# Kernel optimization log

Hardware: AMD Instinct MI355X
Metric: run time of the kernel (lower is better)

Reference implementation:

```python
import jax, jax.numpy as jnp
import numpy as np

B_, T_, N_, C_ = 8, 24, 207, 128      # batch, time (fixed 24), nodes (fixed 207), channels
RED = C_ // 2                          # reducted_size = 64 (Mamba d_model)
DIN = 2 * RED                          # Mamba d_inner (expand=2) = 128
DS, DCONV, DTR = 16, 4, 4              # d_state, d_conv, dt_rank = ceil(64/16)


def _ln(x, w, b, eps=1e-5):
    m = jnp.mean(x, -1, keepdims=True)
    v = jnp.mean((x - m) ** 2, -1, keepdims=True)
    return (x - m) * jax.lax.rsqrt(v + eps) * w + b


def _causal_conv(x, w, b):
    # depthwise causal conv along seq; x: (B,L,D), w: (D,K)
    K = w.shape[1]
    L = x.shape[1]
    xp = jnp.pad(x, ((0, 0), (K - 1, 0), (0, 0)))
    return sum(xp[:, k:k + L, :] * w[:, k] for k in range(K)) + b


def _mamba(h, inproj, conv_w, conv_b, xproj, dtw, dtb, Alog, Dp, outproj):
    # mamba_ssm Mamba(d_model=RED) forward, eval mode
    xz = h @ inproj                                        # (B,L,2*DIN)
    u, z = jnp.split(xz, 2, axis=-1)
    u = jax.nn.silu(_causal_conv(u, conv_w, conv_b))       # (B,L,DIN)
    xdbl = u @ xproj                                       # (B,L,DTR+2*DS)
    dt = jax.nn.softplus(xdbl[..., :DTR] @ dtw + dtb)      # (B,L,DIN)
    Bm = xdbl[..., DTR:DTR + DS]                           # (B,L,DS)
    Cm = xdbl[..., DTR + DS:]                              # (B,L,DS)
    A = -jnp.exp(Alog)                                     # (DIN,DS)

    def step(hs, inp):
        dt_t, B_t, C_t, u_t = inp                          # (B,DIN),(B,DS),(B,DS),(B,DIN)
        hs = hs * jnp.exp(dt_t[..., None] * A) + (dt_t * u_t)[..., None] * B_t[:, None, :]
        return hs, jnp.einsum('bdn,bn->bd', hs, C_t)

    h0 = jnp.zeros((u.shape[0], DIN, DS), u.dtype)
    xs = (dt.swapaxes(0, 1), Bm.swapaxes(0, 1), Cm.swapaxes(0, 1), u.swapaxes(0, 1))
    _, ys = jax.lax.scan(step, h0, xs)                     # (L,B,DIN)
    y = ys.swapaxes(0, 1) + u * Dp
    y = y * jax.nn.silu(z)
    return y @ outproj                                     # (B,L,RED)


def setup_inputs() -> dict:
    key = jax.random.key(0)
    ks = iter(jax.random.split(key, 64))

    def rn(shape, s):
        return jax.random.normal(next(ks), shape, jnp.float32) * s

    inp = {
        "x": jax.random.normal(next(ks), (B_, T_, N_, C_), jnp.float32),
        "qk": jax.random.normal(next(ks), (B_, T_, N_, C_), jnp.float32),
        "in_ln_w": jnp.ones(2 * C_), "in_ln_b": jnp.zeros(2 * C_),
        "in_w": rn((2 * C_, RED), 0.05), "in_b": jnp.zeros(RED),
        "ov_ln_w": jnp.ones(RED), "ov_ln_b": jnp.zeros(RED),
        "ov_w": rn((RED, C_), 0.05), "ov_b": jnp.zeros(C_),
        "o_ln_w": jnp.ones(C_), "o_ln_b": jnp.zeros(C_),
        "o_w": rn((C_, C_), 0.05), "o_b": jnp.zeros(C_),
    }
    for p in ("fw", "bw"):
        inp[p + "_inproj"] = rn((RED, 2 * DIN), 0.05)
        inp[p + "_conv_w"] = rn((DIN, DCONV), 0.2)
        inp[p + "_conv_b"] = jnp.zeros(DIN)
        inp[p + "_xproj"] = rn((DIN, DTR + 2 * DS), 0.05)
        inp[p + "_dtw"] = rn((DTR, DIN), 0.2)
        dt0 = jnp.exp(jax.random.uniform(next(ks), (DIN,)) * (np.log(0.1) - np.log(1e-3)) + np.log(1e-3))
        inp[p + "_dtb"] = jnp.log(jnp.expm1(dt0))          # inverse softplus (mamba dt init)
        inp[p + "_Alog"] = jnp.log(jnp.broadcast_to(jnp.arange(1, DS + 1, dtype=jnp.float32), (DIN, DS)))
        inp[p + "_D"] = jnp.ones(DIN)
        inp[p + "_outproj"] = rn((DIN, RED), 0.05)
    return inp


def reference(x, qk, in_ln_w, in_ln_b, in_w, in_b,
              fw_inproj, fw_conv_w, fw_conv_b, fw_xproj, fw_dtw, fw_dtb, fw_Alog, fw_D, fw_outproj,
              bw_inproj, bw_conv_w, bw_conv_b, bw_xproj, bw_dtw, bw_dtb, bw_Alog, bw_D, bw_outproj,
              ov_ln_w, ov_ln_b, ov_w, ov_b, o_ln_w, o_ln_b, o_w, o_b):
    x_in = x
    h = jnp.concatenate([x, qk], -1).reshape(B_ * T_, N_, 2 * C_)   # 'b t n f -> (b t) n f'
    h = _ln(h, in_ln_w, in_ln_b) @ in_w + in_b                       # (B*T, N, RED)
    h_fw = _mamba(h, fw_inproj, fw_conv_w, fw_conv_b, fw_xproj, fw_dtw, fw_dtb, fw_Alog, fw_D, fw_outproj)
    h_bw = _mamba(h[:, ::-1], bw_inproj, bw_conv_w, bw_conv_b, bw_xproj, bw_dtw, bw_dtb, bw_Alog, bw_D, bw_outproj)[:, ::-1]
    h = h_fw + h_bw
    h = _ln(h, ov_ln_w, ov_ln_b) @ ov_w + ov_b                       # dropout: eval no-op
    h = h.reshape(B_, T_, N_, C_) + x_in                             # '(b t) n f -> b t n f' + residual
    return _ln(h, o_ln_w, o_ln_b) @ o_w + o_b
```

## Files before the change

kernel.cpp:

```cpp
#include <hip/hip_runtime.h>
#include <hip/hip_bf16.h>

#define B__ 8
#define T__ 24
#define N__ 207
#define C__ 128
#define BT_ 192
#define L__ 207
#define RED_ 64
#define DIN_ 128
#define DS_ 16
#define DTR_ 4
#define XD_ 36
#define NC_ 6
#define CHK_ 35
#define NROW_ 39744

#define P_OVLNW 0
#define P_OVLNB 64
#define P_OVB   128
#define P_OLNW  256
#define P_OLNB  384
#define P_OB    512
#define P_INB   640
#define P_LNW   704
#define P_LNB   960
#define P_TOT   1216

using bf16 = __hip_bfloat16;

typedef __attribute__((ext_vector_type(8))) short bf8v;
typedef __attribute__((ext_vector_type(4))) short s4v;
typedef __attribute__((ext_vector_type(4))) float f4v;

__device__ __forceinline__ float ldin(const void* __restrict__ p, int i, int md) {
    if (md) return ((const float*)p)[i];
    return __bfloat162float(((const bf16*)p)[i]);
}
__device__ __forceinline__ float ldbf(const bf16* __restrict__ p, int i) {
    return __bfloat162float(p[i]);
}

__device__ __forceinline__ short f2bf(float f) {
    unsigned u = __builtin_bit_cast(unsigned, f);
    unsigned r = (u + 0x7FFFu + ((u >> 16) & 1u)) >> 16;
    return (short)(unsigned short)r;
}
__device__ __forceinline__ float bfl(short h) {
    return __builtin_bit_cast(float, ((unsigned)(unsigned short)h) << 16);
}

__global__ void k0_detect(const void* __restrict__ lnw, int* __restrict__ mode,
                          int* __restrict__ geo) {
    unsigned short h0 = ((const unsigned short*)lnw)[0];
    *mode = (h0 == 0x3F80u) ? 0 : 1;
    *geo  = 1;
}

__global__ void probe_order_dict() {}
__global__ void probe_order_signature() {}

__global__ __launch_bounds__(256) void k_prep(
    const void* __restrict__ op_fw, const void* __restrict__ op_bw,
    const void* __restrict__ ovw, const void* __restrict__ ow,
    const void* __restrict__ ovlnw, const void* __restrict__ ovlnb,
    const void* __restrict__ ovb,
    const void* __restrict__ olnw, const void* __restrict__ olnb,
    const void* __restrict__ ob,
    const void* __restrict__ inw, const void* __restrict__ inb,
    const void* __restrict__ inlnw, const void* __restrict__ inlnb,
    const void* __restrict__ ipj_fw, const void* __restrict__ ipj_bw,
    const void* __restrict__ cw_fw, const void* __restrict__ cb_fw,
    const void* __restrict__ cw_bw, const void* __restrict__ cb_bw,
    const void* __restrict__ xp_fw, const void* __restrict__ xp_bw,
    const void* __restrict__ Alog_fw, const void* __restrict__ Alog_bw,
    short* __restrict__ w0t_hi, short* __restrict__ w0t_lo,
    short* __restrict__ w2t_hi, short* __restrict__ w2t_lo,
    short* __restrict__ w1t_hi, short* __restrict__ w1t_lo,
    short* __restrict__ ovwt_hi, short* __restrict__ ovwt_lo,
    short* __restrict__ owt_hi, short* __restrict__ owt_lo,
    short* __restrict__ w3t_hi, short* __restrict__ w3t_lo,
    float* __restrict__ cwt, float* __restrict__ cbt,
    float* __restrict__ pars, const int* __restrict__ mode,
    int* __restrict__ geo)
{
    const int md = *mode;
    const int stride = gridDim.x * blockDim.x;
    const int t0 = blockIdx.x * blockDim.x + threadIdx.x;
    for (int i = t0; i < 64*256; i += stride) {
        int c = i >> 8, k = i & 255;
        float wv = ldin(inw, k*64 + c, md);
        short h = f2bf(wv); w0t_hi[i] = h; w0t_lo[i] = f2bf(wv - bfl(h));
    }
    for (int i = t0; i < 2*256*64; i += stride) {
        int dir = i >> 14, c = (i >> 6) & 255, k = i & 63;
        const void* src = dir ? ipj_bw : ipj_fw;
        float wv = ldin(src, k*256 + c, md);
        short h = f2bf(wv); w2t_hi[i] = h; w2t_lo[i] = f2bf(wv - bfl(h));
    }
    for (int i = t0; i < 64*256; i += stride) {
        int c = i >> 8, k = i & 255;
        float wv = (k < 128) ? ldin(op_fw, k*64 + c, md)
                             : ldin(op_bw, (k-128)*64 + c, md);
        short h = f2bf(wv); w1t_hi[i] = h; w1t_lo[i] = f2bf(wv - bfl(h));
    }
    for (int i = t0; i < 128*64; i += stride) {
        int c = i >> 6, k = i & 63;
        float wv = ldin(ovw, k*128 + c, md);
        short h = f2bf(wv); ovwt_hi[i] = h; ovwt_lo[i] = f2bf(wv - bfl(h));
    }
    for (int i = t0; i < 128*128; i += stride) {
        int c = i >> 7, k = i & 127;
        float wv = ldin(ow, k*128 + c, md);
        short h = f2bf(wv); owt_hi[i] = h; owt_lo[i] = f2bf(wv - bfl(h));
    }
    for (int i = t0; i < 2*48*128; i += stride) {
        int dir = i / 6144, rem = i % 6144;
        int c = rem >> 7, k = rem & 127;
        float wv = (c < XD_) ? ldin(dir ? xp_bw : xp_fw, k*XD_ + c, md) : 0.f;
        short h = f2bf(wv); w3t_hi[i] = h; w3t_lo[i] = f2bf(wv - bfl(h));
    }
    for (int i = t0; i < 2*4*128; i += stride) {
        int dir = i >> 9, k = (i >> 7) & 3, d = i & 127;
        cwt[i] = ldin(dir ? cw_bw : cw_fw, d*4 + k, md);
    }
    for (int i = t0; i < 2*128; i += stride) {
        int dir = i >> 7, d = i & 127;
        cbt[i] = ldin(dir ? cb_bw : cb_fw, d, md);
    }
    for (int i = t0; i < 2*DIN_*DS_; i += stride) {
        int dir = i >> 11, rem = i & 2047;
        int d = rem >> 4, s = rem & 15;
        const void* Al = dir ? Alog_bw : Alog_fw;
        float A  = -__expf(ldin(Al, d*DS_ + s, md));
        float A0 = -__expf(ldin(Al, d*DS_ + 0, md));
        float tgt = (float)(s + 1) * A0;
        float tol = 1e-4f * fabsf(tgt) + 1e-6f;
        if (fabsf(A - tgt) > tol) atomicAnd(geo, 0);
    }
    for (int i = t0; i < P_TOT; i += stride) {
        float v;
        if      (i < 64)   v = ldin(ovlnw, i,        md);
        else if (i < 128)  v = ldin(ovlnb, i-64,     md);
        else if (i < 256)  v = ldin(ovb,   i-128,    md);
        else if (i < 384)  v = ldin(olnw,  i-256,    md);
        else if (i < 512)  v = ldin(olnb,  i-384,    md);
        else if (i < 640)  v = ldin(ob,    i-512,    md);
        else if (i < 704)  v = ldin(inb,   i-640,    md);
        else if (i < 960)  v = ldin(inlnw, i-704,    md);
        else               v = ldin(inlnb, i-960,    md);
        pars[i] = v;
    }
}

__global__ __launch_bounds__(64) void k1_mfma(
    const void* __restrict__ x, const void* __restrict__ qk,
    const short* __restrict__ w0t_hi, const short* __restrict__ w0t_lo,
    const float* __restrict__ pars,
    bf16* __restrict__ hbuf, const int* __restrict__ mode)
{
    const int md  = *mode;
    const int l   = threadIdx.x;
    const int lg  = l >> 4;
    const int lc  = l & 15;
    const int wrow = blockIdx.x * 16;
    const int r = wrow + lc;
    const int cb = lg * 32;

    __shared__ __align__(16) short t0h[16][272];
    __shared__ __align__(16) short t0l[16][272];

    const f4v zero = {0.f, 0.f, 0.f, 0.f};

    if (md) {
        float4 vx[8], vq[8];
        const float* spx = (const float*)x  + (size_t)r * C__ + cb;
        const float* spq = (const float*)qk + (size_t)r * C__ + cb;
#pragma unroll
        for (int t = 0; t < 8; ++t) {
            vx[t] = *reinterpret_cast<const float4*>(spx + 4*t);
            vq[t] = *reinterpret_cast<const float4*>(spq + 4*t);
        }
        float s = 0.f, ss = 0.f;
#pragma unroll
        for (int t = 0; t < 8; ++t) {
            s  += vx[t].x + vx[t].y + vx[t].z + vx[t].w
                + vq[t].x + vq[t].y + vq[t].z + vq[t].w;
            ss += vx[t].x*vx[t].x + vx[t].y*vx[t].y + vx[t].z*vx[t].z + vx[t].w*vx[t].w
                + vq[t].x*vq[t].x + vq[t].y*vq[t].y + vq[t].z*vq[t].z + vq[t].w*vq[t].w;
        }
        s  += __shfl_xor(s, 16, 64);  ss += __shfl_xor(ss, 16, 64);
        s  += __shfl_xor(s, 32, 64);  ss += __shfl_xor(ss, 32, 64);
        const float mean = s * (1.f/256.f);
        const float rs   = rsqrtf(ss * (1.f/256.f) - mean*mean + 1e-5f);
#pragma unroll
        for (int t = 0; t < 8; ++t) {
            float vv[4] = {vx[t].x, vx[t].y, vx[t].z, vx[t].w};
            s4v hi, lo;
#pragma unroll
            for (int e = 0; e < 4; ++e) {
                int gc = cb + 4*t + e;
                float a = (vv[e] - mean) * rs * pars[P_LNW + gc] + pars[P_LNB + gc];
                short h = f2bf(a); hi[e] = h; lo[e] = f2bf(a - bfl(h));
            }
            *reinterpret_cast<s4v*>(&t0h[lc][cb + 4*t]) = hi;
            *reinterpret_cast<s4v*>(&t0l[lc][cb + 4*t]) = lo;
        }
#pragma unroll
        for (int t = 0; t < 8; ++t) {
            float vv[4] = {vq[t].x, vq[t].y, vq[t].z, vq[t].w};
            s4v hi, lo;
#pragma unroll
            for (int e = 0; e < 4; ++e) {
                int gc = 128 + cb + 4*t + e;
                float a = (vv[e] - mean) * rs * pars[P_LNW + gc] + pars[P_LNB + gc];
                short h = f2bf(a); hi[e] = h; lo[e] = f2bf(a - bfl(h));
            }
            *reinterpret_cast<s4v*>(&t0h[lc][128 + cb + 4*t]) = hi;
            *reinterpret_cast<s4v*>(&t0l[lc][128 + cb + 4*t]) = lo;
        }
    } else {
        bf8v vx[4], vq[4];
        const short* spx = (const short*)x  + (size_t)r * C__ + cb;
        const short* spq = (const short*)qk + (size_t)r * C__ + cb;
#pragma unroll
        for (int t = 0; t < 4; ++t) {
            vx[t] = *reinterpret_cast<const bf8v*>(spx + 8*t);
            vq[t] = *reinterpret_cast<const bf8v*>(spq + 8*t);
        }
        float s = 0.f, ss = 0.f;
#pragma unroll
        for (int t = 0; t < 4; ++t)
#pragma unroll
            for (int e = 0; e < 8; ++e) {
                float fx = bfl(vx[t][e]); s += fx; ss += fx*fx;
                float fq = bfl(vq[t][e]); s += fq; ss += fq*fq;
            }
        s  += __shfl_xor(s, 16, 64);  ss += __shfl_xor(ss, 16, 64);
        s  += __shfl_xor(s, 32, 64);  ss += __shfl_xor(ss, 32, 64);
        const float mean = s * (1.f/256.f);
        const float rs   = rsqrtf(ss * (1.f/256.f) - mean*mean + 1e-5f);
#pragma unroll
        for (int t = 0; t < 4; ++t)
#pragma unroll
            for (int hh = 0; hh < 2; ++hh) {
                s4v hi, lo;
#pragma unroll
                for (int e = 0; e < 4; ++e) {
                    int gc = cb + 8*t + 4*hh + e;
                    float a = (bfl(vx[t][4*hh+e]) - mean) * rs * pars[P_LNW + gc] + pars[P_LNB + gc];
                    short h = f2bf(a); hi[e] = h; lo[e] = f2bf(a - bfl(h));
                }
                *reinterpret_cast<s4v*>(&t0h[lc][cb + 8*t + 4*hh]) = hi;
                *reinterpret_cast<s4v*>(&t0l[lc][cb + 8*t + 4*hh]) = lo;
            }
#pragma unroll
        for (int t = 0; t < 4; ++t)
#pragma unroll
            for (int hh = 0; hh < 2; ++hh) {
                s4v hi, lo;
#pragma unroll
                for (int e = 0; e < 4; ++e) {
                    int gc = 128 + cb + 8*t + 4*hh + e;
                    float a = (bfl(vq[t][4*hh+e]) - mean) * rs * pars[P_LNW + gc] + pars[P_LNB + gc];
                    short h = f2bf(a); hi[e] = h; lo[e] = f2bf(a - bfl(h));
                }
                *reinterpret_cast<s4v*>(&t0h[lc][128 + cb + 8*t + 4*hh]) = hi;
                *reinterpret_cast<s4v*>(&t0l[lc][128 + cb + 8*t + 4*hh]) = lo;
            }
    }

    f4v acc1[4];
#pragma unroll
    for (int nt = 0; nt < 4; ++nt) acc1[nt] = zero;

#pragma unroll
    for (int p = 0; p < 2; ++p) {
#pragma unroll
        for (int kk = 0; kk < 4; ++kk) {
            bf8v ah = *reinterpret_cast<const bf8v*>(&t0h[lc][p*128 + kk*32 + lg*8]);
            bf8v al = *reinterpret_cast<const bf8v*>(&t0l[lc][p*128 + kk*32 + lg*8]);
#pragma unroll
            for (int nt = 0; nt < 4; ++nt) {
                const int bo = (nt*16 + lc)*256 + p*128 + kk*32 + lg*8;
                bf8v bh = *reinterpret_cast<const bf8v*>(w0t_hi + bo);
                bf8v bl = *reinterpret_cast<const bf8v*>(w0t_lo + bo);
                acc1[nt] = __builtin_amdgcn_mfma_f32_16x16x32_bf16(ah, bl, acc1[nt], 0, 0, 0);
                acc1[nt] = __builtin_amdgcn_mfma_f32_16x16x32_bf16(al, bh, acc1[nt], 0, 0, 0);
                acc1[nt] = __builtin_amdgcn_mfma_f32_16x16x32_bf16(ah, bh, acc1[nt], 0, 0, 0);
            }
        }
    }

    short* hp = (short*)hbuf;
#pragma unroll
    for (int nt = 0; nt < 4; ++nt)
#pragma unroll
        for (int j = 0; j < 4; ++j)
            hp[(size_t)(wrow + lg*4 + j)*RED_ + nt*16 + lc] =
                f2bf(acc1[nt][j] + pars[P_INB + nt*16 + lc]);
}

__global__ __launch_bounds__(64) void k2_mfma(
    const bf16* __restrict__ hbuf,
    const short* __restrict__ w2t_hi, const short* __restrict__ w2t_lo,
    bf16* __restrict__ uraw, bf16* __restrict__ zbuf)
{
    const int l   = threadIdx.x;
    const int lg  = l >> 4;
    const int lc  = l & 15;
    const int wrow = blockIdx.x * 16;
    const int dir  = blockIdx.y >> 1;
    const int nh   = blockIdx.y & 1;

    const short* hp = (const short*)hbuf + (size_t)(wrow + lc) * RED_;
    bf8v ha0 = *reinterpret_cast<const bf8v*>(hp + lg*8);
    bf8v ha1 = *reinterpret_cast<const bf8v*>(hp + 32 + lg*8);

    const f4v zero = {0.f, 0.f, 0.f, 0.f};
    const int g0 = wrow + lg*4;
    const int qg = g0 / 207, ng0 = g0 - qg * 207;

    f4v acc2[8];
#pragma unroll
    for (int nt = 0; nt < 8; ++nt) acc2[nt] = zero;
#pragma unroll
    for (int nt = 0; nt < 8; ++nt) {
        const int ntg = nh*8 + nt;
        const int co = dir*16384 + (ntg*16 + lc)*64;
        bf8v bh0 = *reinterpret_cast<const bf8v*>(w2t_hi + co + lg*8);
        bf8v bl0 = *reinterpret_cast<const bf8v*>(w2t_lo + co + lg*8);
        bf8v bh1 = *reinterpret_cast<const bf8v*>(w2t_hi + co + 32 + lg*8);
        bf8v bl1 = *reinterpret_cast<const bf8v*>(w2t_lo + co + 32 + lg*8);
        acc2[nt] = __builtin_amdgcn_mfma_f32_16x16x32_bf16(ha0, bl0, acc2[nt], 0, 0, 0);
        acc2[nt] = __builtin_amdgcn_mfma_f32_16x16x32_bf16(ha0, bh0, acc2[nt], 0, 0, 0);
        acc2[nt] = __builtin_amdgcn_mfma_f32_16x16x32_bf16(ha1, bl1, acc2[nt], 0, 0, 0);
        acc2[nt] = __builtin_amdgcn_mfma_f32_16x16x32_bf16(ha1, bh1, acc2[nt], 0, 0, 0);
    }
    bf16* __restrict__ dst = nh ? zbuf : uraw;
#pragma unroll
    for (int j = 0; j < 4; ++j) {
        int ng = ng0 + j, qq = qg;
        if (ng >= 207) { ng -= 207; ++qq; }
        const int ro = dir ? ((192 + qq)*207 + (206 - ng)) : (qq*207 + ng);
#pragma unroll
        for (int nt = 0; nt < 8; ++nt) {
            const int c = nt*16 + lc;
            dst[(size_t)ro*DIN_ + c] = __float2bfloat16(acc2[nt][j]);
        }
    }
}

__global__ __launch_bounds__(64) void k34_mfma(
    const bf16* __restrict__ uraw,
    const float* __restrict__ cwt, const float* __restrict__ cbt,
    const short* __restrict__ w3t_hi, const short* __restrict__ w3t_lo,
    bf16* __restrict__ ubuf, float* __restrict__ xdbl)
{
    const int l   = threadIdx.x;
    const int lg  = l >> 4;
    const int lc  = l & 15;
    const int wrow = blockIdx.x * 16;
    const int dir  = wrow / NROW_;
    const int r    = wrow + lc;
    const int m    = (r - dir * NROW_) % 207;

    __shared__ __align__(16) short uhh[16][136];
    __shared__ __align__(16) short ull[16][136];

    const float* __restrict__ cw = cwt + dir * 512;
    const float* __restrict__ cb = cbt + dir * 128;
    const int c0 = lg * 32;

#pragma unroll
    for (int t = 0; t < 4; ++t) {
        const int cc = c0 + t*8;
        float s[8];
#pragma unroll
        for (int e = 0; e < 8; ++e) s[e] = cb[cc + e];
#pragma unroll
        for (int k = 0; k < 3; ++k) {
            if (m - 3 + k >= 0) {
                bf8v v = *reinterpret_cast<const bf8v*>(
                    (const short*)uraw + (size_t)(r - 3 + k)*DIN_ + cc);
#pragma unroll
                for (int e = 0; e < 8; ++e) s[e] += bfl(v[e]) * cw[k*128 + cc + e];
            }
        }
        {
            bf8v v = *reinterpret_cast<const bf8v*>(
                (const short*)uraw + (size_t)r*DIN_ + cc);
#pragma unroll
            for (int e = 0; e < 8; ++e) s[e] += bfl(v[e]) * cw[3*128 + cc + e];
        }
        s4v h0, h1, l0, l1;
        bf8v uo;
#pragma unroll
        for (int e = 0; e < 8; ++e) {
            float u = s[e] / (1.f + __expf(-s[e]));
            short h = f2bf(u);
            short lo = f2bf(u - bfl(h));
            uo[e] = h;
            if (e < 4) { h0[e] = h; l0[e] = lo; }
            else       { h1[e-4] = h; l1[e-4] = lo; }
        }
        *reinterpret_cast<s4v*>(&uhh[lc][cc])     = h0;
        *reinterpret_cast<s4v*>(&uhh[lc][cc + 4]) = h1;
        *reinterpret_cast<s4v*>(&ull[lc][cc])     = l0;
        *reinterpret_cast<s4v*>(&ull[lc][cc + 4]) = l1;
        *reinterpret_cast<bf8v*>((short*)ubuf + (size_t)r*DIN_ + cc) = uo;
    }

    const f4v zero = {0.f, 0.f, 0.f, 0.f};
    f4v acc[3];
#pragma unroll
    for (int nt = 0; nt < 3; ++nt) acc[nt] = zero;
    const int wb = dir * 6144;
#pragma unroll
    for (int kk = 0; kk < 4; ++kk) {
        bf8v ah = *reinterpret_cast<const bf8v*>(&uhh[lc][kk*32 + lg*8]);
        bf8v al = *reinterpret_cast<const bf8v*>(&ull[lc][kk*32 + lg*8]);
#pragma unroll
        for (int nt = 0; nt < 3; ++nt) {
            const int bo = wb + (nt*16 + lc)*128 + kk*32 + lg*8;
            bf8v bh = *reinterpret_cast<const bf8v*>(w3t_hi + bo);
            bf8v bl = *reinterpret_cast<const bf8v*>(w3t_lo + bo);
            acc[nt] = __builtin_amdgcn_mfma_f32_16x16x32_bf16(ah, bl, acc[nt], 0, 0, 0);
            acc[nt] = __builtin_amdgcn_mfma_f32_16x16x32_bf16(al, bh, acc[nt], 0, 0, 0);
            acc[nt] = __builtin_amdgcn_mfma_f32_16x16x32_bf16(ah, bh, acc[nt], 0, 0, 0);
        }
    }
#pragma unroll
    for (int nt = 0; nt < 3; ++nt) {
        const int c = nt*16 + lc;
        if (c < XD_) {
#pragma unroll
            for (int j = 0; j < 4; ++j)
                xdbl[(size_t)(wrow + lg*4 + j)*XD_ + c] = acc[nt][j];
        }
    }
}

__global__ __launch_bounds__(128) void k5a_local(
    const float* __restrict__ xdbl,
    const bf16* __restrict__ ubuf,
    float* __restrict__ h_end, float* __restrict__ sumdt,
    const void* __restrict__ dtw_fw, const void* __restrict__ dtb_fw,
    const void* __restrict__ Alog_fw,
    const void* __restrict__ dtw_bw, const void* __restrict__ dtb_bw,
    const void* __restrict__ Alog_bw,
    const int* __restrict__ mode, const int* __restrict__ geo)
{
    const int md = *mode;
    const int c = blockIdx.x, q = blockIdx.y, dir = blockIdx.z;
    const int d = threadIdx.x;
    const void* __restrict__ dtw  = dir ? dtw_bw  : dtw_fw;
    const void* __restrict__ dtbp = dir ? dtb_bw  : dtb_fw;
    const void* __restrict__ Alog = dir ? Alog_bw : Alog_fw;
    const float w0 = ldin(dtw, 0*DIN_ + d, md), w1 = ldin(dtw, 1*DIN_ + d, md);
    const float w2 = ldin(dtw, 2*DIN_ + d, md), w3 = ldin(dtw, 3*DIN_ + d, md);
    const float dtb = ldin(dtbp, d, md);
    float st[DS_];
#pragma unroll
    for (int s = 0; s < DS_; ++s) st[s] = 0.f;
    float sdt = 0.f;
    const int seq = dir*BT_ + q;
    const int m0 = c * CHK_;
    if (*geo) {
        const float A0 = -__expf(ldin(Alog, d*DS_ + 0, md));
        for (int m = m0; m < m0 + CHK_; ++m) {
            const float* __restrict__ xd = xdbl + (seq*L__ + m)*XD_;
            float4 xt = *reinterpret_cast<const float4*>(xd);
            float dtp = xt.x*w0 + xt.y*w1 + xt.z*w2 + xt.w*w3 + dtb;
            float dt = (dtp > 15.f) ? dtp : __logf(1.f + __expf(dtp));
            sdt += dt;
            float u = ldbf(ubuf, (seq*L__ + m)*DIN_ + d);
            float du = dt * u;
            float bb[DS_];
#pragma unroll
            for (int t = 0; t < 4; ++t) {
                float4 v = *reinterpret_cast<const float4*>(xd + DTR_ + 4*t);
                bb[4*t] = v.x; bb[4*t+1] = v.y; bb[4*t+2] = v.z; bb[4*t+3] = v.w;
            }
            float e1 = __expf(dt * A0);
            float pw = 1.f;
#pragma unroll
            for (int s = 0; s < DS_; ++s) {
                pw *= e1;
                st[s] = st[s]*pw + du*bb[s];
            }
        }
    } else {
        float A[DS_];
#pragma unroll
        for (int s = 0; s < DS_; ++s) A[s] = -__expf(ldin(Alog, d*DS_ + s, md));
        for (int m = m0; m < m0 + CHK_; ++m) {
            const float* __restrict__ xd = xdbl + (seq*L__ + m)*XD_;
            float4 xt = *reinterpret_cast<const float4*>(xd);
            float dtp = xt.x*w0 + xt.y*w1 + xt.z*w2 + xt.w*w3 + dtb;
            float dt = (dtp > 15.f) ? dtp : log1pf(__expf(dtp));
            sdt += dt;
            float u = ldbf(ubuf, (seq*L__ + m)*DIN_ + d);
            float du = dt * u;
            float bb[DS_];
#pragma unroll
            for (int t = 0; t < 4; ++t) {
                float4 v = *reinterpret_cast<const float4*>(xd + DTR_ + 4*t);
                bb[4*t] = v.x; bb[4*t+1] = v.y; bb[4*t+2] = v.z; bb[4*t+3] = v.w;
            }
#pragma unroll
            for (int s = 0; s < DS_; ++s)
                st[s] = st[s]*__expf(dt*A[s]) + du*bb[s];
        }
    }
    float* __restrict__ he = h_end + (size_t)(seq*5 + c)*(DIN_*DS_) + d*DS_;
#pragma unroll
    for (int t = 0; t < 4; ++t) {
        float4 v; v.x = st[4*t]; v.y = st[4*t+1]; v.z = st[4*t+2]; v.w = st[4*t+3];
        *reinterpret_cast<float4*>(he + 4*t) = v;
    }
    sumdt[(seq*5 + c)*DIN_ + d] = sdt;
}

__global__ __launch_bounds__(128) void k5c_scan(
    const float* __restrict__ xdbl,
    const bf16* __restrict__ zbuf,
    bf16* __restrict__ ubuf,
    const float* __restrict__ h_end, const float* __restrict__ sumdt,
    const void* __restrict__ dtw_fw, const void* __restrict__ dtb_fw,
    const void* __restrict__ Alog_fw, const void* __restrict__ D_fw,
    const void* __restrict__ dtw_bw, const void* __restrict__ dtb_bw,
    const void* __restrict__ Alog_bw, const void* __restrict__ D_bw,
    const int* __restrict__ mode, const int* __restrict__ geo)
{
    const int md = *mode;
    const int c = blockIdx.x, q = blockIdx.y, dir = blockIdx.z;
    const int d = threadIdx.x;
    const void* __restrict__ dtw  = dir ? dtw_bw  : dtw_fw;
    const void* __restrict__ dtbp = dir ? dtb_bw  : dtb_fw;
    const void* __restrict__ Alog = dir ? Alog_bw : Alog_fw;
    const void* __restrict__ Dp   = dir ? D_bw    : D_fw;
    const float w0 = ldin(dtw, 0*DIN_ + d, md), w1 = ldin(dtw, 1*DIN_ + d, md);
    const float w2 = ldin(dtw, 2*DIN_ + d, md), w3 = ldin(dtw, 3*DIN_ + d, md);
    const float dtb = ldin(dtbp, d, md), Dv = ldin(Dp, d, md);
    const int seq = dir*BT_ + q;
    const int m0 = c * CHK_;
    const int m1 = (m0 + CHK_ < L__) ? (m0 + CHK_) : L__;

    float st[DS_];
#pragma unroll
    for (int s = 0; s < DS_; ++s) st[s] = 0.f;

    if (*geo) {
        const float A0 = -__expf(ldin(Alog, d*DS_ + 0, md));
        for (int j = 0; j < c; ++j) {
            float sd = sumdt[(seq*5 + j)*DIN_ + d];
            const float* __restrict__ he = h_end + (size_t)(seq*5 + j)*(DIN_*DS_) + d*DS_;
            float hv[DS_];
#pragma unroll
            for (int t = 0; t < 4; ++t) {
                float4 v = *reinterpret_cast<const float4*>(he + 4*t);
                hv[4*t] = v.x; hv[4*t+1] = v.y; hv[4*t+2] = v.z; hv[4*t+3] = v.w;
            }
            float e1 = __expf(A0 * sd);
            float pw = 1.f;
#pragma unroll
            for (int s = 0; s < DS_; ++s) {
                pw *= e1;
                st[s] = st[s]*pw + hv[s];
            }
        }
        for (int m = m0; m < m1; ++m) {
            const float* __restrict__ xd = xdbl + (seq*L__ + m)*XD_;
            float4 xt = *reinterpret_cast<const float4*>(xd);
            float dtp = xt.x*w0 + xt.y*w1 + xt.z*w2 + xt.w*w3 + dtb;
            float dt = (dtp > 15.f) ? dtp : __logf(1.f + __expf(dtp));
            const int uidx = (seq*L__ + m)*DIN_ + d;
            float u = ldbf(ubuf, uidx);
            float du = dt * u;
            float bb[DS_], cc[DS_];
#pragma unroll
            for (int t = 0; t < 4; ++t) {
                float4 v = *reinterpret_cast<const float4*>(xd + DTR_ + 4*t);
                bb[4*t] = v.x; bb[4*t+1] = v.y; bb[4*t+2] = v.z; bb[4*t+3] = v.w;
                float4 w = *reinterpret_cast<const float4*>(xd + DTR_ + DS_ + 4*t);
                cc[4*t] = w.x; cc[4*t+1] = w.y; cc[4*t+2] = w.z; cc[4*t+3] = w.w;
            }
            float e1 = __expf(dt * A0);
            float pw = 1.f;
            float y = 0.f;
#pragma unroll
            for (int s = 0; s < DS_; ++s) {
                pw *= e1;
                st[s] = st[s]*pw + du*bb[s];
                y += st[s]*cc[s];
            }
            y += u * Dv;
            float z = ldbf(zbuf, uidx);
            y *= z / (1.f + __expf(-z));
            ubuf[uidx] = __float2bfloat16(y);
        }
    } else {
        float A[DS_];
#pragma unroll
        for (int s = 0; s < DS_; ++s) A[s] = -__expf(ldin(Alog, d*DS_ + s, md));
        for (int j = 0; j < c; ++j) {
            float sd = sumdt[(seq*5 + j)*DIN_ + d];
            const float* __restrict__ he = h_end + (size_t)(seq*5 + j)*(DIN_*DS_) + d*DS_;
            float hv[DS_];
#pragma unroll
            for (int t = 0; t < 4; ++t) {
                float4 v = *reinterpret_cast<const float4*>(he + 4*t);
                hv[4*t] = v.x; hv[4*t+1] = v.y; hv[4*t+2] = v.z; hv[4*t+3] = v.w;
            }
#pragma unroll
            for (int s = 0; s < DS_; ++s)
                st[s] = st[s]*__expf(A[s]*sd) + hv[s];
        }
        for (int m = m0; m < m1; ++m) {
            const float* __restrict__ xd = xdbl + (seq*L__ + m)*XD_;
            float4 xt = *reinterpret_cast<const float4*>(xd);
            float dtp = xt.x*w0 + xt.y*w1 + xt.z*w2 + xt.w*w3 + dtb;
            float dt = (dtp > 15.f) ? dtp : log1pf(__expf(dtp));
            const int uidx = (seq*L__ + m)*DIN_ + d;
            float u = ldbf(ubuf, uidx);
            float du = dt * u;
            float bb[DS_], cc[DS_];
#pragma unroll
            for (int t = 0; t < 4; ++t) {
                float4 v = *reinterpret_cast<const float4*>(xd + DTR_ + 4*t);
                bb[4*t] = v.x; bb[4*t+1] = v.y; bb[4*t+2] = v.z; bb[4*t+3] = v.w;
                float4 w = *reinterpret_cast<const float4*>(xd + DTR_ + DS_ + 4*t);
                cc[4*t] = w.x; cc[4*t+1] = w.y; cc[4*t+2] = w.z; cc[4*t+3] = w.w;
            }
            float y = 0.f;
#pragma unroll
            for (int s = 0; s < DS_; ++s) {
                st[s] = st[s]*__expf(dt*A[s]) + du*bb[s];
                y += st[s]*cc[s];
            }
            y += u * Dv;
            float z = ldbf(zbuf, uidx);
            y *= z / (1.f + __expf(-z));
            ubuf[uidx] = __float2bfloat16(y);
        }
    }
}

__global__ __launch_bounds__(64) void k6_mfma(
    const bf16* __restrict__ ubuf,
    const short* __restrict__ w1t_hi, const short* __restrict__ w1t_lo,
    const short* __restrict__ ovwt_hi, const short* __restrict__ ovwt_lo,
    const short* __restrict__ owt_hi, const short* __restrict__ owt_lo,
    const float* __restrict__ pars,
    const void* __restrict__ x, void* __restrict__ out,
    const int* __restrict__ mode)
{
    const int md  = *mode;
    const int l   = threadIdx.x;
    const int lg  = l >> 4;
    const int lc  = l & 15;
    const int wrow = blockIdx.x * 16;

    __shared__ __align__(16) short t1h[16][72];
    __shared__ __align__(16) short t1l[16][72];
    __shared__ __align__(16) short t2h[16][136];
    __shared__ __align__(16) short t2l[16][136];

    const f4v zero = {0.f, 0.f, 0.f, 0.f};

    const int ra = wrow + lc;
    const int qa = ra / 207, na = ra - qa * 207;
    const short* yfp = (const short*)ubuf + ra * 128 + lg * 8;
    const short* ybp = (const short*)ubuf + ((192 + qa) * 207 + (206 - na)) * 128 + lg * 8;

    f4v acc[4];
#pragma unroll
    for (int nt = 0; nt < 4; ++nt) acc[nt] = zero;

#pragma unroll
    for (int ks = 0; ks < 8; ++ks) {
        const short* ap = (ks < 4) ? (yfp + ks * 32) : (ybp + (ks - 4) * 32);
        bf8v a = *reinterpret_cast<const bf8v*>(ap);
#pragma unroll
        for (int nt = 0; nt < 4; ++nt) {
            const int bo = (nt * 16 + lc) * 256 + ks * 32 + lg * 8;
            bf8v bh = *reinterpret_cast<const bf8v*>(w1t_hi + bo);
            bf8v bl = *reinterpret_cast<const bf8v*>(w1t_lo + bo);
            acc[nt] = __builtin_amdgcn_mfma_f32_16x16x32_bf16(a, bl, acc[nt], 0, 0, 0);
            acc[nt] = __builtin_amdgcn_mfma_f32_16x16x32_bf16(a, bh, acc[nt], 0, 0, 0);
        }
    }

    {
        float sv[8];
#pragma unroll
        for (int i = 0; i < 8; ++i) sv[i] = 0.f;
#pragma unroll
        for (int nt = 0; nt < 4; ++nt)
#pragma unroll
            for (int j = 0; j < 4; ++j) { float v = acc[nt][j]; sv[j] += v; sv[4+j] += v*v; }
#pragma unroll
        for (int off = 8; off >= 1; off >>= 1)
#pragma unroll
            for (int i = 0; i < 8; ++i) sv[i] += __shfl_xor(sv[i], off, 64);
#pragma unroll
        for (int j = 0; j < 4; ++j) {
            float mean = sv[j] * (1.f/64.f);
            float var  = sv[4+j] * (1.f/64.f) - mean*mean;
            float rs   = rsqrtf(var + 1e-5f);
#pragma unroll
            for (int nt = 0; nt < 4; ++nt) {
                int c = nt*16 + lc;
                float t1 = (acc[nt][j] - mean) * rs * pars[c] + pars[64 + c];
                short h = f2bf(t1);
                t1h[lg*4+j][c] = h;
                t1l[lg*4+j][c] = f2bf(t1 - bfl(h));
            }
        }
    }

    f4v acc2[8];
#pragma unroll
    for (int nt = 0; nt < 8; ++nt) acc2[nt] = zero;
#pragma unroll
    for (int ks = 0; ks < 2; ++ks) {
        bf8v a  = *reinterpret_cast<const bf8v*>(&t1h[lc][ks*32 + lg*8]);
        bf8v al = *reinterpret_cast<const bf8v*>(&t1l[lc][ks*32 + lg*8]);
#pragma unroll
        for (int nt = 0; nt < 8; ++nt) {
            const int bo = (nt*16 + lc) * 64 + ks*32 + lg*8;
            bf8v bh = *reinterpret_cast<const bf8v*>(ovwt_hi + bo);
            bf8v bl = *reinterpret_cast<const bf8v*>(ovwt_lo + bo);
            acc2[nt] = __builtin_amdgcn_mfma_f32_16x16x32_bf16(a,  bh, acc2[nt], 0, 0, 0);
            acc2[nt] = __builtin_amdgcn_mfma_f32_16x16x32_bf16(a,  bl, acc2[nt], 0, 0, 0);
            acc2[nt] = __builtin_amdgcn_mfma_f32_16x16x32_bf16(al, bh, acc2[nt], 0, 0, 0);
        }
    }

    const int rc = wrow + lg*4;
#pragma unroll
    for (int nt = 0; nt < 8; ++nt)
#pragma unroll
        for (int j = 0; j < 4; ++j) acc2[nt][j] += pars[128 + nt*16 + lc];
    if (md) {
        const float* xf = (const float*)x;
#pragma unroll
        for (int nt = 0; nt < 8; ++nt)
#pragma unroll
            for (int j = 0; j < 4; ++j)
                acc2[nt][j] += xf[(rc + j)*128 + nt*16 + lc];
    } else {
        const bf16* xb = (const bf16*)x;
#pragma unroll
        for (int nt = 0; nt < 8; ++nt)
#pragma unroll
            for (int j = 0; j < 4; ++j)
                acc2[nt][j] += ldbf(xb, (rc + j)*128 + nt*16 + lc);
    }

    {
        float sv[8];
#pragma unroll
        for (int i = 0; i < 8; ++i) sv[i] = 0.f;
#pragma unroll
        for (int nt = 0; nt < 8; ++nt)
#pragma unroll
            for (int j = 0; j < 4; ++j) { float v = acc2[nt][j]; sv[j] += v; sv[4+j] += v*v; }
#pragma unroll
        for (int off = 8; off >= 1; off >>= 1)
#pragma unroll
            for (int i = 0; i < 8; ++i) sv[i] += __shfl_xor(sv[i], off, 64);
#pragma unroll
        for (int j = 0; j < 4; ++j) {
            float mean = sv[j] * (1.f/128.f);
            float var  = sv[4+j] * (1.f/128.f) - mean*mean;
            float rs   = rsqrtf(var + 1e-5f);
#pragma unroll
            for (int nt = 0; nt < 8; ++nt) {
                int c = nt*16 + lc;
                float t2 = (acc2[nt][j] - mean) * rs * pars[256 + c] + pars[384 + c];
                short h = f2bf(t2);
                t2h[lg*4+j][c] = h;
                t2l[lg*4+j][c] = f2bf(t2 - bfl(h));
            }
        }
    }

    f4v acc3[8];
#pragma unroll
    for (int nt = 0; nt < 8; ++nt) acc3[nt] = zero;
#pragma unroll
    for (int ks = 0; ks < 4; ++ks) {
        bf8v a  = *reinterpret_cast<const bf8v*>(&t2h[lc][ks*32 + lg*8]);
        bf8v al = *reinterpret_cast<const bf8v*>(&t2l[lc][ks*32 + lg*8]);
#pragma unroll
        for (int nt = 0; nt < 8; ++nt) {
            const int bo = (nt*16 + lc) * 128 + ks*32 + lg*8;
            bf8v bh = *reinterpret_cast<const bf8v*>(owt_hi + bo);
            bf8v bl = *reinterpret_cast<const bf8v*>(owt_lo + bo);
            acc3[nt] = __builtin_amdgcn_mfma_f32_16x16x32_bf16(a,  bh, acc3[nt], 0, 0, 0);
            acc3[nt] = __builtin_amdgcn_mfma_f32_16x16x32_bf16(a,  bl, acc3[nt], 0, 0, 0);
            acc3[nt] = __builtin_amdgcn_mfma_f32_16x16x32_bf16(al, bh, acc3[nt], 0, 0, 0);
        }
    }
    if (md) {
        float* of = (float*)out;
#pragma unroll
        for (int nt = 0; nt < 8; ++nt)
#pragma unroll
            for (int j = 0; j < 4; ++j) {
                int c = nt*16 + lc;
                of[(rc + j)*128 + c] = acc3[nt][j] + pars[512 + c];
            }
    } else {
        bf16* ob_ = (bf16*)out;
#pragma unroll
        for (int nt = 0; nt < 8; ++nt)
#pragma unroll
            for (int j = 0; j < 4; ++j) {
                int c = nt*16 + lc;
                ob_[(rc + j)*128 + c] = __float2bfloat16(acc3[nt][j] + pars[512 + c]);
            }
    }
}

extern "C" void kernel_launch(void* const* d_in, const int* in_sizes, int n_in,
                              void* d_out, int out_size, void* d_ws, size_t ws_size,
                              hipStream_t stream)
{
    const bool sig = (n_in > 6) && (in_sizes[6] == 16384);

    const void *x, *qk, *inlnw, *inlnb, *inw, *inb;
    const void *ovlnw, *ovlnb, *ovw, *ovb, *olnw, *olnb, *ow, *ob;
    const void *fw_inproj, *fw_convw, *fw_convb, *fw_xproj, *fw_dtw, *fw_dtb,
               *fw_Alog, *fw_D, *fw_outproj;
    const void *bw_inproj, *bw_convw, *bw_convb, *bw_xproj, *bw_dtw, *bw_dtb,
               *bw_Alog, *bw_D, *bw_outproj;

    x = d_in[0]; qk = d_in[1]; inlnw = d_in[2]; inlnb = d_in[3];
    inw = d_in[4]; inb = d_in[5];
    if (!sig) {
        ovlnw = d_in[6];  ovlnb = d_in[7];  ovw = d_in[8];  ovb = d_in[9];
        olnw  = d_in[10]; olnb  = d_in[11]; ow  = d_in[12]; ob  = d_in[13];
        fw_inproj = d_in[14]; fw_convw = d_in[15]; fw_convb = d_in[16];
        fw_xproj = d_in[17]; fw_dtw = d_in[18]; fw_dtb = d_in[19];
        fw_Alog = d_in[20]; fw_D = d_in[21]; fw_outproj = d_in[22];
        bw_inproj = d_in[23]; bw_convw = d_in[24]; bw_convb = d_in[25];
        bw_xproj = d_in[26]; bw_dtw = d_in[27]; bw_dtb = d_in[28];
        bw_Alog = d_in[29]; bw_D = d_in[30]; bw_outproj = d_in[31];
    } else {
        fw_inproj = d_in[6];  fw_convw = d_in[7];  fw_convb = d_in[8];
        fw_xproj = d_in[9];  fw_dtw = d_in[10]; fw_dtb = d_in[11];
        fw_Alog = d_in[12]; fw_D = d_in[13]; fw_outproj = d_in[14];
        bw_inproj = d_in[15]; bw_convw = d_in[16]; bw_convb = d_in[17];
        bw_xproj = d_in[18]; bw_dtw = d_in[19]; bw_dtb = d_in[20];
        bw_Alog = d_in[21]; bw_D = d_in[22]; bw_outproj = d_in[23];
        ovlnw = d_in[24]; ovlnb = d_in[25]; ovw = d_in[26]; ovb = d_in[27];
        olnw  = d_in[28]; olnb  = d_in[29]; ow  = d_in[30]; ob  = d_in[31];
    }

    char* ws = (char*)d_ws;
    int*   mode = (int*)(ws);
    int*   geo  = (int*)(ws + 8);
    float* sumdt = (float*)(ws + 16);
    short* w0t_hi  = (short*)(ws + 983056);
    short* w0t_lo  = (short*)(ws + 1015824);
    short* w2t_hi  = (short*)(ws + 1048592);
    short* w2t_lo  = (short*)(ws + 1114128);
    bf16*  uraw = (bf16*)(ws + 5087248);
    float* h_end = (float*)(ws + 5087248);
    bf16*  zbuf = (bf16*)(ws + 25436176);
    bf16*  ubuf = (bf16*)(ws + 45785104);
    float* xdbl = (float*)(ws + 66134032);
    bf16*  hbuf = (bf16*)(ws + 66134032);
    short* w1t_hi  = (short*)(ws + 77580304);
    short* w1t_lo  = (short*)(ws + 77613072);
    short* ovwt_hi = (short*)(ws + 77645840);
    short* ovwt_lo = (short*)(ws + 77662224);
    short* owt_hi  = (short*)(ws + 77678608);
    short* owt_lo  = (short*)(ws + 77711376);
    float* pars    = (float*)(ws + 77744144);
    short* w3t_hi  = (short*)(ws + 77749008);
    short* w3t_lo  = (short*)(ws + 77773584);
    float* cwt     = (float*)(ws + 77798160);
    float* cbt     = (float*)(ws + 77802256);

    if (sig) probe_order_signature<<<1, 64, 0, stream>>>();
    else     probe_order_dict<<<1, 64, 0, stream>>>();

    k0_detect<<<1, 1, 0, stream>>>(inlnw, mode, geo);
    k_prep<<<40, 256, 0, stream>>>(
        fw_outproj, bw_outproj, ovw, ow,
        ovlnw, ovlnb, ovb, olnw, olnb, ob,
        inw, inb, inlnw, inlnb, fw_inproj, bw_inproj,
        fw_convw, fw_convb, bw_convw, bw_convb, fw_xproj, bw_xproj,
        fw_Alog, bw_Alog,
        w0t_hi, w0t_lo, w2t_hi, w2t_lo,
        w1t_hi, w1t_lo, ovwt_hi, ovwt_lo, owt_hi, owt_lo,
        w3t_hi, w3t_lo, cwt, cbt, pars, mode, geo);
    k1_mfma<<<dim3(2484), 64, 0, stream>>>(
        x, qk, w0t_hi, w0t_lo, pars, hbuf, mode);
    k2_mfma<<<dim3(2484, 4), 64, 0, stream>>>(
        hbuf, w2t_hi, w2t_lo, uraw, zbuf);
    k34_mfma<<<dim3(4968), 64, 0, stream>>>(
        uraw, cwt, cbt, w3t_hi, w3t_lo, ubuf, xdbl);
    k5a_local<<<dim3(NC_-1, BT_, 2), 128, 0, stream>>>(
        xdbl, ubuf, h_end, sumdt,
        fw_dtw, fw_dtb, fw_Alog,
        bw_dtw, bw_dtb, bw_Alog, mode, geo);
    k5c_scan<<<dim3(NC_, BT_, 2), 128, 0, stream>>>(
        xdbl, zbuf, ubuf, h_end, sumdt,
        fw_dtw, fw_dtb, fw_Alog, fw_D,
        bw_dtw, bw_dtb, bw_Alog, bw_D, mode, geo);
    k6_mfma<<<dim3(2484), 64, 0, stream>>>(
        ubuf, w1t_hi, w1t_lo, ovwt_hi, ovwt_lo, owt_hi, owt_lo, pars,
        x, d_out, mode);
}
```

Measured before the change: 398.4 us.

## Split SSM state dimension across two threads per channel in scan kernels

The chunked selective-scan kernels now assign two threads per inner channel, each owning 8 of the 16 state entries, and launch twice as many blocks. In the geometric-A path each half seeds its power chain at e1 or e1^9 via repeated squaring. The output dot product is combined with a lane shuffle, and only one lane writes y. This doubles thread-level parallelism and halves per-thread register state and serial latency, at the cost of duplicated dt/softplus and u loads in both lanes.

New measurement: 417.3 us. +4.7%, slower.

```diff
diff --git a/kernel.cpp b/kernel.cpp
--- a/kernel.cpp
+++ b/kernel.cpp
@@ -452,17 +452,20 @@
     const int* __restrict__ mode, const int* __restrict__ geo)
 {
     const int md = *mode;
-    const int c = blockIdx.x, q = blockIdx.y, dir = blockIdx.z;
-    const int d = threadIdx.x;
+    const int c = blockIdx.x, q = blockIdx.y;
+    const int dir = blockIdx.z >> 1, dh = blockIdx.z & 1;
+    const int tid = threadIdx.x;
+    const int d  = dh*64 + (tid >> 1);
+    const int sh = tid & 1;
     const void* __restrict__ dtw  = dir ? dtw_bw  : dtw_fw;
     const void* __restrict__ dtbp = dir ? dtb_bw  : dtb_fw;
     const void* __restrict__ Alog = dir ? Alog_bw : Alog_fw;
     const float w0 = ldin(dtw, 0*DIN_ + d, md), w1 = ldin(dtw, 1*DIN_ + d, md);
     const float w2 = ldin(dtw, 2*DIN_ + d, md), w3 = ldin(dtw, 3*DIN_ + d, md);
     const float dtb = ldin(dtbp, d, md);
-    float st[DS_];
-#pragma unroll
-    for (int s = 0; s < DS_; ++s) st[s] = 0.f;
+    float st[8];
+#pragma unroll
+    for (int s = 0; s < 8; ++s) st[s] = 0.f;
     float sdt = 0.f;
     const int seq = dir*BT_ + q;
     const int m0 = c * CHK_;
@@ -476,24 +479,23 @@
             sdt += dt;
             float u = ldbf(ubuf, (seq*L__ + m)*DIN_ + d);
             float du = dt * u;
-            float bb[DS_];
-#pragma unroll
-            for (int t = 0; t < 4; ++t) {
-                float4 v = *reinterpret_cast<const float4*>(xd + DTR_ + 4*t);
-                bb[4*t] = v.x; bb[4*t+1] = v.y; bb[4*t+2] = v.z; bb[4*t+3] = v.w;
-            }
+            float4 b0 = *reinterpret_cast<const float4*>(xd + DTR_ + sh*8);
+            float4 b1 = *reinterpret_cast<const float4*>(xd + DTR_ + sh*8 + 4);
+            float bb[8] = {b0.x,b0.y,b0.z,b0.w,b1.x,b1.y,b1.z,b1.w};
             float e1 = __expf(dt * A0);
-            float pw = 1.f;
-#pragma unroll
-            for (int s = 0; s < DS_; ++s) {
+            float e2 = e1*e1, e4 = e2*e2, e8 = e4*e4;
+            float pw = sh ? e8*e1 : e1;
+            st[0] = st[0]*pw + du*bb[0];
+#pragma unroll
+            for (int s = 1; s < 8; ++s) {
                 pw *= e1;
                 st[s] = st[s]*pw + du*bb[s];
             }
         }
     } else {
-        float A[DS_];
-#pragma unroll
-        for (int s = 0; s < DS_; ++s) A[s] = -__expf(ldin(Alog, d*DS_ + s, md));
+        float A[8];
+#pragma unroll
+        for (int s = 0; s < 8; ++s) A[s] = -__expf(ldin(Alog, d*DS_ + sh*8 + s, md));
         for (int m = m0; m < m0 + CHK_; ++m) {
             const float* __restrict__ xd = xdbl + (seq*L__ + m)*XD_;
             float4 xt = *reinterpret_cast<const float4*>(xd);
@@ -502,24 +504,22 @@
             sdt += dt;
             float u = ldbf(ubuf, (seq*L__ + m)*DIN_ + d);
             float du = dt * u;
-            float bb[DS_];
-#pragma unroll
-            for (int t = 0; t < 4; ++t) {
-                float4 v = *reinterpret_cast<const float4*>(xd + DTR_ + 4*t);
-                bb[4*t] = v.x; bb[4*t+1] = v.y; bb[4*t+2] = v.z; bb[4*t+3] = v.w;
-            }
-#pragma unroll
-            for (int s = 0; s < DS_; ++s)
+            float4 b0 = *reinterpret_cast<const float4*>(xd + DTR_ + sh*8);
+            float4 b1 = *reinterpret_cast<const float4*>(xd + DTR_ + sh*8 + 4);
+            float bb[8] = {b0.x,b0.y,b0.z,b0.w,b1.x,b1.y,b1.z,b1.w};
+#pragma unroll
+            for (int s = 0; s < 8; ++s)
                 st[s] = st[s]*__expf(dt*A[s]) + du*bb[s];
         }
     }
-    float* __restrict__ he = h_end + (size_t)(seq*5 + c)*(DIN_*DS_) + d*DS_;
-#pragma unroll
-    for (int t = 0; t < 4; ++t) {
-        float4 v; v.x = st[4*t]; v.y = st[4*t+1]; v.z = st[4*t+2]; v.w = st[4*t+3];
-        *reinterpret_cast<float4*>(he + 4*t) = v;
-    }
-    sumdt[(seq*5 + c)*DIN_ + d] = sdt;
+    float* __restrict__ he = h_end + (size_t)(seq*5 + c)*(DIN_*DS_) + d*DS_ + sh*8;
+    {
+        float4 v0; v0.x = st[0]; v0.y = st[1]; v0.z = st[2]; v0.w = st[3];
+        float4 v1; v1.x = st[4]; v1.y = st[5]; v1.z = st[6]; v1.w = st[7];
+        *reinterpret_cast<float4*>(he)     = v0;
+        *reinterpret_cast<float4*>(he + 4) = v1;
+    }
+    if (sh == 0) sumdt[(seq*5 + c)*DIN_ + d] = sdt;
 }
 
 __global__ __launch_bounds__(128) void k5c_scan(
@@ -534,8 +534,11 @@
     const int* __restrict__ mode, const int* __restrict__ geo)
 {
     const int md = *mode;
-    const int c = blockIdx.x, q = blockIdx.y, dir = blockIdx.z;
-    const int d = threadIdx.x;
+    const int c = blockIdx.x, q = blockIdx.y;
+    const int dir = blockIdx.z >> 1, dh = blockIdx.z & 1;
+    const int tid = threadIdx.x;
+    const int d  = dh*64 + (tid >> 1);
+    const int sh = tid & 1;
     const void* __restrict__ dtw  = dir ? dtw_bw  : dtw_fw;
     const void* __restrict__ dtbp = dir ? dtb_bw  : dtb_fw;
     const void* __restrict__ Alog = dir ? Alog_bw : Alog_fw;
@@ -547,25 +550,25 @@
     const int m0 = c * CHK_;
     const int m1 = (m0 + CHK_ < L__) ? (m0 + CHK_) : L__;
 
-    float st[DS_];
-#pragma unroll
-    for (int s = 0; s < DS_; ++s) st[s] = 0.f;
+    float st[8];
+#pragma unroll
+    for (int s = 0; s < 8; ++s) st[s] = 0.f;
 
     if (*geo) {
         const float A0 = -__expf(ldin(Alog, d*DS_ + 0, md));
         for (int j = 0; j < c; ++j) {
             float sd = sumdt[(seq*5 + j)*DIN_ + d];
-            const float* __restrict__ he = h_end + (size_t)(seq*5 + j)*(DIN_*DS_) + d*DS_;
-            float hv[DS_];
-#pragma unroll
-            for (int t = 0; t < 4; ++t) {
-                float4 v = *reinterpret_cast<const float4*>(he + 4*t);
-                hv[4*t] = v.x; hv[4*t+1] = v.y; hv[4*t+2] = v.z; hv[4*t+3] = v.w;
-            }
+            const float* __restrict__ he =
+                h_end + (size_t)(seq*5 + j)*(DIN_*DS_) + d*DS_ + sh*8;
+            float4 v0 = *reinterpret_cast<const float4*>(he);
+            float4 v1 = *reinterpret_cast<const float4*>(he + 4);
+            float hv[8] = {v0.x,v0.y,v0.z,v0.w,v1.x,v1.y,v1.z,v1.w};
             float e1 = __expf(A0 * sd);
-            float pw = 1.f;
-#pragma unroll
-            for (int s = 0; s < DS_; ++s) {
+            float e2 = e1*e1, e4 = e2*e2, e8 = e4*e4;
+            float pw = sh ? e8*e1 : e1;
+            st[0] = st[0]*pw + hv[0];
+#pragma unroll
+            for (int s = 1; s < 8; ++s) {
                 pw *= e1;
                 st[s] = st[s]*pw + hv[s];
             }
@@ -578,43 +581,45 @@
             const int uidx = (seq*L__ + m)*DIN_ + d;
             float u = ldbf(ubuf, uidx);
             float du = dt * u;
-            float bb[DS_], cc[DS_];
-#pragma unroll
-            for (int t = 0; t < 4; ++t) {
-                float4 v = *reinterpret_cast<const float4*>(xd + DTR_ + 4*t);
-                bb[4*t] = v.x; bb[4*t+1] = v.y; bb[4*t+2] = v.z; bb[4*t+3] = v.w;
-                float4 w = *reinterpret_cast<const float4*>(xd + DTR_ + DS_ + 4*t);
-                cc[4*t] = w.x; cc[4*t+1] = w.y; cc[4*t+2] = w.z; cc[4*t+3] = w.w;
-            }
+            float4 b0 = *reinterpret_cast<const float4*>(xd + DTR_ + sh*8);
+            float4 b1 = *reinterpret_cast<const float4*>(xd + DTR_ + sh*8 + 4);
+            float bb[8] = {b0.x,b0.y,b0.z,b0.w,b1.x,b1.y,b1.z,b1.w};
+            float4 c0v = *reinterpret_cast<const float4*>(xd + DTR_ + DS_ + sh*8);
+            float4 c1v = *reinterpret_cast<const float4*>(xd + DTR_ + DS_ + sh*8 + 4);
+            float cc2[8] = {c0v.x,c0v.y,c0v.z,c0v.w,c1v.x,c1v.y,c1v.z,c1v.w};
             float e1 = __expf(dt * A0);
-            float pw = 1.f;
+            float e2 = e1*e1, e4 = e2*e2, e8 = e4*e4;
+            float pw = sh ? e8*e1 : e1;
             float y = 0.f;
-#pragma unroll
-            for (int s = 0; s < DS_; ++s) {
+            st[0] = st[0]*pw + du*bb[0];
+            y += st[0]*cc2[0];
+#pragma unroll
+            for (int s = 1; s < 8; ++s) {
                 pw *= e1;
                 st[s] = st[s]*pw + du*bb[s];
-                y += st[s]*cc[s];
-            }
-            y += u * Dv;
-            float z = ldbf(zbuf, uidx);
-            y *= z / (1.f + __expf(-z));
-            ubuf[uidx] = __float2bfloat16(y);
+                y += st[s]*cc2[s];
+            }
+            y += __shfl_xor(y, 1, 64);
+            if (sh == 0) {
+                y += u * Dv;
+                float z = ldbf(zbuf, uidx);
+                y *= z / (1.f + __expf(-z));
+                ubuf[uidx] = __float2bfloat16(y);
+            }
         }
     } else {
-        float A[DS_];
-#pragma unroll
-        for (int s = 0; s < DS_; ++s) A[s] = -__expf(ldin(Alog, d*DS_ + s, md));
+        float A[8];
+#pragma unroll
+        for (int s = 0; s < 8; ++s) A[s] = -__expf(ldin(Alog, d*DS_ + sh*8 + s, md));
         for (int j = 0; j < c; ++j) {
             float sd = sumdt[(seq*5 + j)*DIN_ + d];
-            const float* __restrict__ he = h_end + (size_t)(seq*5 + j)*(DIN_*DS_) + d*DS_;
-            float hv[DS_];
-#pragma unroll
-            for (int t = 0; t < 4; ++t) {
-                float4 v = *reinterpret_cast<const float4*>(he + 4*t);
-                hv[4*t] = v.x; hv[4*t+1] = v.y; hv[4*t+2] = v.z; hv[4*t+3] = v.w;
-            }
-#pragma unroll
-            for (int s = 0; s < DS_; ++s)
+            const float* __restrict__ he =
+                h_end + (size_t)(seq*5 + j)*(DIN_*DS_) + d*DS_ + sh*8;
+            float4 v0 = *reinterpret_cast<const float4*>(he);
+            float4 v1 = *reinterpret_cast<const float4*>(he + 4);
+            float hv[8] = {v0.x,v0.y,v0.z,v0.w,v1.x,v1.y,v1.z,v1.w};
+#pragma unroll
+            for (int s = 0; s < 8; ++s)
                 st[s] = st[s]*__expf(A[s]*sd) + hv[s];
         }
         for (int m = m0; m < m1; ++m) {
@@ -625,24 +630,25 @@
             const int uidx = (seq*L__ + m)*DIN_ + d;
             float u = ldbf(ubuf, uidx);
             float du = dt * u;
-            float bb[DS_], cc[DS_];
-#pragma unroll
-            for (int t = 0; t < 4; ++t) {
-                float4 v = *reinterpret_cast<const float4*>(xd + DTR_ + 4*t);
-                bb[4*t] = v.x; bb[4*t+1] = v.y; bb[4*t+2] = v.z; bb[4*t+3] = v.w;
-                float4 w = *reinterpret_cast<const float4*>(xd + DTR_ + DS_ + 4*t);
-                cc[4*t] = w.x; cc[4*t+1] = w.y; cc[4*t+2] = w.z; cc[4*t+3] = w.w;
-            }
+            float4 b0 = *reinterpret_cast<const float4*>(xd + DTR_ + sh*8);
+            float4 b1 = *reinterpret_cast<const float4*>(xd + DTR_ + sh*8 + 4);
+            float bb[8] = {b0.x,b0.y,b0.z,b0.w,b1.x,b1.y,b1.z,b1.w};
+            float4 c0v = *reinterpret_cast<const float4*>(xd + DTR_ + DS_ + sh*8);
+            float4 c1v = *reinterpret_cast<const float4*>(xd + DTR_ + DS_ + sh*8 + 4);
+            float cc2[8] = {c0v.x,c0v.y,c0v.z,c0v.w,c1v.x,c1v.y,c1v.z,c1v.w};
             float y = 0.f;
 #pragma unroll
-            for (int s = 0; s < DS_; ++s) {
+            for (int s = 0; s < 8; ++s) {
                 st[s] = st[s]*__expf(dt*A[s]) + du*bb[s];
-                y += st[s]*cc[s];
-            }
-            y += u * Dv;
-            float z = ldbf(zbuf, uidx);
-            y *= z / (1.f + __expf(-z));
-            ubuf[uidx] = __float2bfloat16(y);
+                y += st[s]*cc2[s];
+            }
+            y += __shfl_xor(y, 1, 64);
+            if (sh == 0) {
+                y += u * Dv;
+                float z = ldbf(zbuf, uidx);
+                y *= z / (1.f + __expf(-z));
+                ubuf[uidx] = __float2bfloat16(y);
+            }
         }
     }
 }
@@ -905,11 +911,11 @@
         hbuf, w2t_hi, w2t_lo, uraw, zbuf);
     k34_mfma<<<dim3(4968), 64, 0, stream>>>(
         uraw, cwt, cbt, w3t_hi, w3t_lo, ubuf, xdbl);
-    k5a_local<<<dim3(NC_-1, BT_, 2), 128, 0, stream>>>(
+    k5a_local<<<dim3(NC_-1, BT_, 4), 128, 0, stream>>>(
         xdbl, ubuf, h_end, sumdt,
         fw_dtw, fw_dtb, fw_Alog,
         bw_dtw, bw_dtb, bw_Alog, mode, geo);
-    k5c_scan<<<dim3(NC_, BT_, 2), 128, 0, stream>>>(
+    k5c_scan<<<dim3(NC_, BT_, 4), 128, 0, stream>>>(
         xdbl, zbuf, ubuf, h_end, sumdt,
         fw_dtw, fw_dtb, fw_Alog, fw_D,
         bw_dtw, bw_dtb, bw_Alog, bw_D, mode, geo);
```
